# Kernel optimization log

Hardware: AMD Instinct MI355X
Metric: run time of the kernel (lower is better)

## Reference

```python
import jax, jax.numpy as jnp
import numpy as np

HIDDEN = 2048
VOCAB = 50257


def setup_inputs() -> dict:
    key = jax.random.key(0)
    ks = jax.random.split(key, 9)
    s = 0.02
    return {
        "token": jax.random.randint(ks[0], (1,), 0, VOCAB, dtype=jnp.int32),
        "hidden": jax.random.normal(ks[1], (1, 1, HIDDEN), dtype=jnp.float32),
        "emb": jax.random.normal(ks[2], (VOCAB, HIDDEN), dtype=jnp.float32) * s,
        "w_ih": jax.random.normal(ks[3], (3 * HIDDEN, HIDDEN), dtype=jnp.float32) * s,
        "w_hh": jax.random.normal(ks[4], (3 * HIDDEN, HIDDEN), dtype=jnp.float32) * s,
        "b_ih": jax.random.normal(ks[5], (3 * HIDDEN,), dtype=jnp.float32) * s,
        "b_hh": jax.random.normal(ks[6], (3 * HIDDEN,), dtype=jnp.float32) * s,
        "w_out": jax.random.normal(ks[7], (VOCAB, HIDDEN), dtype=jnp.float32) * s,
        "b_out": jax.random.normal(ks[8], (VOCAB,), dtype=jnp.float32) * s,
    }


def reference(token, hidden, emb, w_ih, w_hh, b_ih, b_hh, w_out, b_out):
    # embedding lookup + view(1,1,-1) + ReLU  -> x: [H]
    x = jax.nn.relu(emb[token].reshape(-1))
    h = hidden.reshape(-1)  # [H]
    # single GRU step (PyTorch gate order: r, z, n; separate input/hidden biases)
    gi = w_ih @ x + b_ih  # [3H]
    gh = w_hh @ h + b_hh  # [3H]
    i_r, i_z, i_n = jnp.split(gi, 3)
    h_r, h_z, h_n = jnp.split(gh, 3)
    r = jax.nn.sigmoid(i_r + h_r)
    z = jax.nn.sigmoid(i_z + h_z)
    n = jnp.tanh(i_n + r * h_n)
    h_new = (1.0 - z) * n + z * h  # [H]
    # output projection + log-softmax over vocab (dim=1 of [1, V])
    logits = w_out @ h_new + b_out  # [V]
    out = jax.nn.log_softmax(logits)[None, :]  # [1, V]
    return out, h_new.reshape(1, 1, -1)
```

## Files before the change

### kernel.cpp

```cpp
#include <hip/hip_runtime.h>
#include <math.h>

#define H 2048
#define G 6144
#define V 50257

#define WS_HNEW  0
#define WS_LOGIT 2048
#define WS_PMAX  53248
#define WS_PSUM  53376
#define NPART    128
#define NB2      6283
#define WS_PMAX2 53248
#define WS_PSUM2 59648
#define WS_FUSED_END 66048

typedef float f4 __attribute__((ext_vector_type(4)));

__device__ __forceinline__ float waveReduceSum(float v) {
  #pragma unroll
  for (int off = 32; off > 0; off >>= 1) v += __shfl_down(v, off, 64);
  return v;
}
__device__ __forceinline__ float waveReduceMax(float v) {
  #pragma unroll
  for (int off = 32; off > 0; off >>= 1) v = fmaxf(v, __shfl_down(v, off, 64));
  return v;
}
__device__ __forceinline__ float sigmoidf(float x) {
  return 1.f / (1.f + expf(-x));
}

__global__ __launch_bounds__(256) void gru_kernel(
    const int* __restrict__ token, const float* __restrict__ hidden,
    const float* __restrict__ emb, const float* __restrict__ w_ih,
    const float* __restrict__ w_hh, const float* __restrict__ b_ih,
    const float* __restrict__ b_hh, float* __restrict__ ws,
    float* __restrict__ out) {
  const int wave = threadIdx.x >> 6;
  const int lane = threadIdx.x & 63;
  const int li   = wave >> 1;
  const int side = wave & 1;
  const int i = blockIdx.x * 2 + li;
  __shared__ float sums[2][2][3];

  const f4* v4 = side ? (const f4*)hidden
                      : (const f4*)(emb + (size_t)token[0] * H);
  const float* wmat = side ? w_hh : w_ih;
  const f4* w_r = (const f4*)(wmat + (size_t)i * H);
  const f4* w_z = (const f4*)(wmat + (size_t)(H + i) * H);
  const f4* w_n = (const f4*)(wmat + (size_t)(2 * H + i) * H);

  float sr = 0.f, sz = 0.f, sn = 0.f;
  #pragma unroll
  for (int k = 0; k < 8; ++k) {
    const int idx = k * 64 + lane;
    f4 xv = v4[idx];
    if (!side) {
      xv.x = fmaxf(xv.x, 0.f); xv.y = fmaxf(xv.y, 0.f);
      xv.z = fmaxf(xv.z, 0.f); xv.w = fmaxf(xv.w, 0.f);
    }
    f4 a;
    a = w_r[idx]; sr += a.x*xv.x + a.y*xv.y + a.z*xv.z + a.w*xv.w;
    a = w_z[idx]; sz += a.x*xv.x + a.y*xv.y + a.z*xv.z + a.w*xv.w;
    a = w_n[idx]; sn += a.x*xv.x + a.y*xv.y + a.z*xv.z + a.w*xv.w;
  }
  sr = waveReduceSum(sr);
  sz = waveReduceSum(sz);
  sn = waveReduceSum(sn);
  if (lane == 0) {
    sums[li][side][0] = sr;
    sums[li][side][1] = sz;
    sums[li][side][2] = sn;
  }
  __syncthreads();
  if (side == 0 && lane == 0) {
    const float s_ir = sums[li][0][0], s_hr = sums[li][1][0];
    const float s_iz = sums[li][0][1], s_hz = sums[li][1][1];
    const float s_in = sums[li][0][2], s_hn = sums[li][1][2];
    const float r = sigmoidf(s_ir + b_ih[i] + s_hr + b_hh[i]);
    const float z = sigmoidf(s_iz + b_ih[H + i] + s_hz + b_hh[H + i]);
    const float n = tanhf(s_in + b_ih[2 * H + i] + r * (s_hn + b_hh[2 * H + i]));
    const float hn = (1.f - z) * n + z * hidden[i];
    ws[WS_HNEW + i] = hn;
    out[V + i] = hn;
  }
}

__global__ __launch_bounds__(256) void logits_kernel(
    const float* __restrict__ w_out, const float* __restrict__ b_out,
    float* __restrict__ ws, int write_partials) {
  const int wave = threadIdx.x >> 6;
  const int lane = threadIdx.x & 63;
  const int row0 = blockIdx.x * 8 + wave * 2;
  const int valid0 = (row0 < V);
  const int valid1 = (row0 + 1 < V);
  const int r0 = valid0 ? row0 : 0;
  const int r1 = valid1 ? row0 + 1 : 0;

  const f4* h4 = (const f4*)(ws + WS_HNEW);
  f4 hv[8];
  #pragma unroll
  for (int k = 0; k < 8; ++k) hv[k] = h4[k * 64 + lane];

  const f4* w0 = (const f4*)(w_out + (size_t)r0 * H);
  const f4* w1 = (const f4*)(w_out + (size_t)r1 * H);
  float s0 = 0.f, s1 = 0.f;
  #pragma unroll
  for (int k = 0; k < 8; ++k) {
    const int idx = k * 64 + lane;
    f4 a0 = __builtin_nontemporal_load(w0 + idx);
    f4 a1 = __builtin_nontemporal_load(w1 + idx);
    s0 += a0.x*hv[k].x + a0.y*hv[k].y + a0.z*hv[k].z + a0.w*hv[k].w;
    s1 += a1.x*hv[k].x + a1.y*hv[k].y + a1.z*hv[k].z + a1.w*hv[k].w;
  }
  s0 = waveReduceSum(s0);
  s1 = waveReduceSum(s1);

  __shared__ float lv[8];
  if (lane == 0) {
    const float l0 = s0 + b_out[r0];
    const float l1 = s1 + b_out[r1];
    lv[wave * 2]     = valid0 ? l0 : -INFINITY;
    lv[wave * 2 + 1] = valid1 ? l1 : -INFINITY;
    if (valid0) ws[WS_LOGIT + row0] = l0;
    if (valid1) ws[WS_LOGIT + row0 + 1] = l1;
  }
  if (!write_partials) return;
  __syncthreads();
  if (threadIdx.x == 0) {
    float m = -INFINITY;
    #pragma unroll
    for (int j = 0; j < 8; ++j) m = fmaxf(m, lv[j]);
    float s = 0.f;
    #pragma unroll
    for (int j = 0; j < 8; ++j) s += expf(lv[j] - m);
    ws[WS_PMAX2 + blockIdx.x] = m;
    ws[WS_PSUM2 + blockIdx.x] = s;
  }
}

__global__ __launch_bounds__(256) void writeout_big_kernel(
    const float* __restrict__ ws, float* __restrict__ out, int nb) {
  __shared__ float sred[4];
  __shared__ float sM, sLse;
  const int wave = threadIdx.x >> 6;
  const int lane = threadIdx.x & 63;
  float m = -INFINITY;
  for (int j = threadIdx.x; j < nb; j += 256) m = fmaxf(m, ws[WS_PMAX2 + j]);
  m = waveReduceMax(m);
  if (lane == 0) sred[wave] = m;
  __syncthreads();
  if (threadIdx.x == 0)
    sM = fmaxf(fmaxf(sred[0], sred[1]), fmaxf(sred[2], sred[3]));
  __syncthreads();
  const float M = sM;
  float s = 0.f;
  for (int j = threadIdx.x; j < nb; j += 256)
    s += ws[WS_PSUM2 + j] * expf(ws[WS_PMAX2 + j] - M);
  s = waveReduceSum(s);
  __syncthreads();
  if (lane == 0) sred[wave] = s;
  __syncthreads();
  if (threadIdx.x == 0)
    sLse = M + logf(sred[0] + sred[1] + sred[2] + sred[3]);
  __syncthreads();
  const float lse = sLse;
  const int i = blockIdx.x * 256 + threadIdx.x;
  if (i < V) out[i] = ws[WS_LOGIT + i] - lse;
}

__global__ __launch_bounds__(256) void partial_kernel(float* __restrict__ ws) {
  __shared__ float sred[4];
  __shared__ float sbmax;
  const int wave = threadIdx.x >> 6;
  const int lane = threadIdx.x & 63;
  float m = -INFINITY;
  for (int i = blockIdx.x * 256 + threadIdx.x; i < V; i += NPART * 256)
    m = fmaxf(m, ws[WS_LOGIT + i]);
  m = waveReduceMax(m);
  if (lane == 0) sred[wave] = m;
  __syncthreads();
  if (threadIdx.x == 0)
    sbmax = fmaxf(fmaxf(sred[0], sred[1]), fmaxf(sred[2], sred[3]));
  __syncthreads();
  const float M = sbmax;
  float s = 0.f;
  for (int i = blockIdx.x * 256 + threadIdx.x; i < V; i += NPART * 256)
    s += expf(ws[WS_LOGIT + i] - M);
  s = waveReduceSum(s);
  __syncthreads();
  if (lane == 0) sred[wave] = s;
  __syncthreads();
  if (threadIdx.x == 0) {
    ws[WS_PMAX + blockIdx.x] = M;
    ws[WS_PSUM + blockIdx.x] = sred[0] + sred[1] + sred[2] + sred[3];
  }
}

__global__ __launch_bounds__(256) void writeout_kernel(
    const float* __restrict__ ws, float* __restrict__ out) {
  __shared__ float pm[NPART], psv[NPART];
  __shared__ float sM[2], sS[2];
  __shared__ float sLse;
  const int tid = threadIdx.x;
  if (tid < NPART) {
    pm[tid]  = ws[WS_PMAX + tid];
    psv[tid] = ws[WS_PSUM + tid];
  }
  __syncthreads();
  if (tid < NPART) {
    float m = waveReduceMax(pm[tid]);
    if ((tid & 63) == 0) sM[tid >> 6] = m;
  }
  __syncthreads();
  const float M = fmaxf(sM[0], sM[1]);
  if (tid < NPART) {
    float e = psv[tid] * expf(pm[tid] - M);
    e = waveReduceSum(e);
    if ((tid & 63) == 0) sS[tid >> 6] = e;
  }
  __syncthreads();
  if (tid == 0) sLse = M + logf(sS[0] + sS[1]);
  __syncthreads();
  const float lse = sLse;
  const int i = blockIdx.x * 256 + tid;
  if (i < V) out[i] = ws[WS_LOGIT + i] - lse;
}

extern "C" void kernel_launch(void* const* d_in, const int* in_sizes, int n_in,
                              void* d_out, int out_size, void* d_ws, size_t ws_size,
                              hipStream_t stream) {
  const int*   token  = (const int*)  d_in[0];
  const float* hidden = (const float*)d_in[1];
  const float* emb    = (const float*)d_in[2];
  const float* w_ih   = (const float*)d_in[3];
  const float* w_hh   = (const float*)d_in[4];
  const float* b_ih   = (const float*)d_in[5];
  const float* b_hh   = (const float*)d_in[6];
  const float* w_out  = (const float*)d_in[7];
  const float* b_out  = (const float*)d_in[8];
  float* out = (float*)d_out;
  float* ws  = (float*)d_ws;

  const int fused = (ws_size >= (size_t)WS_FUSED_END * sizeof(float));

  gru_kernel<<<H / 2, 256, 0, stream>>>(token, hidden, emb, w_ih, w_hh,
                                        b_ih, b_hh, ws, out);
  logits_kernel<<<NB2, 256, 0, stream>>>(w_out, b_out, ws, fused);
  if (fused) {
    writeout_big_kernel<<<(V + 255) / 256, 256, 0, stream>>>(ws, out, NB2);
  } else {
    partial_kernel<<<NPART, 256, 0, stream>>>(ws);
    writeout_kernel<<<(V + 255) / 256, 256, 0, stream>>>(ws, out);
  }
}
```

Baseline: 744.7 us.

## Fuse log-softmax finalize into logits kernel via last-block atomic counter

The logits kernel now processes 16 rows per block (4 per wave) and drops the nontemporal loads. After each block writes its partial max and sum, it increments an atomic counter, and the last block merges all partials with an online max/sum and writes the normalized output with vectorized stores. This removes the separate writeout launch. In exchange, the final write of all 50K outputs runs on a single block.

```diff
diff --git a/kernel.cpp b/kernel.cpp
--- a/kernel.cpp
+++ b/kernel.cpp
@@ -2,18 +2,19 @@
 #include <math.h>
 
 #define H 2048
-#define G 6144
 #define V 50257
+#define RPB 16
+#define NB2 ((V + RPB - 1) / RPB)
+#define NPART 128
 
 #define WS_HNEW  0
 #define WS_LOGIT 2048
 #define WS_PMAX  53248
 #define WS_PSUM  53376
-#define NPART    128
-#define NB2      6283
 #define WS_PMAX2 53248
-#define WS_PSUM2 59648
-#define WS_FUSED_END 66048
+#define WS_PSUM2 56448
+#define WS_CNT   59648
+#define WS_END   59712
 
 typedef float f4 __attribute__((ext_vector_type(4)));
 
@@ -37,6 +38,7 @@
     const float* __restrict__ w_hh, const float* __restrict__ b_ih,
     const float* __restrict__ b_hh, float* __restrict__ ws,
     float* __restrict__ out) {
+  if (blockIdx.x == 0 && threadIdx.x == 0) *(int*)(ws + WS_CNT) = 0;
   const int wave = threadIdx.x >> 6;
   const int lane = threadIdx.x & 63;
   const int li   = wave >> 1;
@@ -87,87 +89,119 @@
   }
 }
 
-__global__ __launch_bounds__(256) void logits_kernel(
+__global__ __launch_bounds__(256, 4) void logits_kernel(
     const float* __restrict__ w_out, const float* __restrict__ b_out,
-    float* __restrict__ ws, int write_partials) {
+    float* __restrict__ ws, float* __restrict__ out, int fused) {
   const int wave = threadIdx.x >> 6;
   const int lane = threadIdx.x & 63;
-  const int row0 = blockIdx.x * 8 + wave * 2;
-  const int valid0 = (row0 < V);
-  const int valid1 = (row0 + 1 < V);
-  const int r0 = valid0 ? row0 : 0;
-  const int r1 = valid1 ? row0 + 1 : 0;
+  const int row0 = blockIdx.x * RPB + wave * 4;
+  int   r[4];
+  int   valid[4];
+  #pragma unroll
+  for (int j = 0; j < 4; ++j) {
+    valid[j] = (row0 + j < V);
+    r[j] = valid[j] ? row0 + j : 0;
+  }
 
   const f4* h4 = (const f4*)(ws + WS_HNEW);
   f4 hv[8];
   #pragma unroll
   for (int k = 0; k < 8; ++k) hv[k] = h4[k * 64 + lane];
 
-  const f4* w0 = (const f4*)(w_out + (size_t)r0 * H);
-  const f4* w1 = (const f4*)(w_out + (size_t)r1 * H);
-  float s0 = 0.f, s1 = 0.f;
+  const f4* wp0 = (const f4*)(w_out + (size_t)r[0] * H);
+  const f4* wp1 = (const f4*)(w_out + (size_t)r[1] * H);
+  const f4* wp2 = (const f4*)(w_out + (size_t)r[2] * H);
+  const f4* wp3 = (const f4*)(w_out + (size_t)r[3] * H);
+  float s0 = 0.f, s1 = 0.f, s2 = 0.f, s3 = 0.f;
   #pragma unroll
   for (int k = 0; k < 8; ++k) {
     const int idx = k * 64 + lane;
-    f4 a0 = __builtin_nontemporal_load(w0 + idx);
-    f4 a1 = __builtin_nontemporal_load(w1 + idx);
+    f4 a0 = wp0[idx];
+    f4 a1 = wp1[idx];
+    f4 a2 = wp2[idx];
+    f4 a3 = wp3[idx];
     s0 += a0.x*hv[k].x + a0.y*hv[k].y + a0.z*hv[k].z + a0.w*hv[k].w;
     s1 += a1.x*hv[k].x + a1.y*hv[k].y + a1.z*hv[k].z + a1.w*hv[k].w;
+    s2 += a2.x*hv[k].x + a2.y*hv[k].y + a2.z*hv[k].z + a2.w*hv[k].w;
+    s3 += a3.x*hv[k].x + a3.y*hv[k].y + a3.z*hv[k].z + a3.w*hv[k].w;
   }
   s0 = waveReduceSum(s0);
   s1 = waveReduceSum(s1);
-
-  __shared__ float lv[8];
+  s2 = waveReduceSum(s2);
+  s3 = waveReduceSum(s3);
+
+  __shared__ float lv[RPB];
   if (lane == 0) {
-    const float l0 = s0 + b_out[r0];
-    const float l1 = s1 + b_out[r1];
-    lv[wave * 2]     = valid0 ? l0 : -INFINITY;
-    lv[wave * 2 + 1] = valid1 ? l1 : -INFINITY;
-    if (valid0) ws[WS_LOGIT + row0] = l0;
-    if (valid1) ws[WS_LOGIT + row0 + 1] = l1;
-  }
-  if (!write_partials) return;
-  __syncthreads();
+    float sv[4] = {s0, s1, s2, s3};
+    #pragma unroll
+    for (int j = 0; j < 4; ++j) {
+      const float l = sv[j] + b_out[r[j]];
+      lv[wave * 4 + j] = valid[j] ? l : -INFINITY;
+      if (valid[j]) ws[WS_LOGIT + row0 + j] = l;
+    }
+  }
+  if (!fused) return;
+  __syncthreads();
+
+  __shared__ int sLast;
   if (threadIdx.x == 0) {
     float m = -INFINITY;
     #pragma unroll
-    for (int j = 0; j < 8; ++j) m = fmaxf(m, lv[j]);
-    float s = 0.f;
-    #pragma unroll
-    for (int j = 0; j < 8; ++j) s += expf(lv[j] - m);
+    for (int j = 0; j < RPB; ++j) m = fmaxf(m, lv[j]);
+    float ss = 0.f;
+    #pragma unroll
+    for (int j = 0; j < RPB; ++j) ss += expf(lv[j] - m);
     ws[WS_PMAX2 + blockIdx.x] = m;
-    ws[WS_PSUM2 + blockIdx.x] = s;
-  }
-}
-
-__global__ __launch_bounds__(256) void writeout_big_kernel(
-    const float* __restrict__ ws, float* __restrict__ out, int nb) {
-  __shared__ float sred[4];
-  __shared__ float sM, sLse;
-  const int wave = threadIdx.x >> 6;
-  const int lane = threadIdx.x & 63;
-  float m = -INFINITY;
-  for (int j = threadIdx.x; j < nb; j += 256) m = fmaxf(m, ws[WS_PMAX2 + j]);
-  m = waveReduceMax(m);
-  if (lane == 0) sred[wave] = m;
-  __syncthreads();
-  if (threadIdx.x == 0)
-    sM = fmaxf(fmaxf(sred[0], sred[1]), fmaxf(sred[2], sred[3]));
-  __syncthreads();
-  const float M = sM;
-  float s = 0.f;
-  for (int j = threadIdx.x; j < nb; j += 256)
-    s += ws[WS_PSUM2 + j] * expf(ws[WS_PMAX2 + j] - M);
-  s = waveReduceSum(s);
-  __syncthreads();
-  if (lane == 0) sred[wave] = s;
-  __syncthreads();
-  if (threadIdx.x == 0)
-    sLse = M + logf(sred[0] + sred[1] + sred[2] + sred[3]);
+    ws[WS_PSUM2 + blockIdx.x] = ss;
+    __threadfence();
+    const int old = atomicAdd((int*)(ws + WS_CNT), 1);
+    sLast = (old == NB2 - 1);
+  }
+  __syncthreads();
+  if (!sLast) return;
+
+  __threadfence();
+  float m = -INFINITY, ss = 0.f;
+  for (int j = threadIdx.x; j < NB2; j += 256) {
+    const float pm = ws[WS_PMAX2 + j];
+    const float ps = ws[WS_PSUM2 + j];
+    const float nm = fmaxf(m, pm);
+    ss = ss * expf(m - nm) + ps * expf(pm - nm);
+    m = nm;
+  }
+  #pragma unroll
+  for (int off = 32; off > 0; off >>= 1) {
+    const float m2 = __shfl_down(m, off, 64);
+    const float ss2 = __shfl_down(ss, off, 64);
+    const float nm = fmaxf(m, m2);
+    ss = ss * expf(m - nm) + ss2 * expf(m2 - nm);
+    m = nm;
+  }
+  __shared__ float redM[4], redS[4];
+  __shared__ float sLse;
+  if (lane == 0) { redM[wave] = m; redS[wave] = ss; }
+  __syncthreads();
+  if (threadIdx.x == 0) {
+    float M = -INFINITY, S = 0.f;
+    #pragma unroll
+    for (int w = 0; w < 4; ++w) {
+      const float nm = fmaxf(M, redM[w]);
+      S = S * expf(M - nm) + redS[w] * expf(redM[w] - nm);
+      M = nm;
+    }
+    sLse = M + logf(S);
+  }
   __syncthreads();
   const float lse = sLse;
-  const int i = blockIdx.x * 256 + threadIdx.x;
-  if (i < V) out[i] = ws[WS_LOGIT + i] - lse;
+  const int nvec = V / 4;
+  const f4* lg4 = (const f4*)(ws + WS_LOGIT);
+  f4* out4 = (f4*)out;
+  for (int j = threadIdx.x; j < nvec; j += 256) {
+    f4 l = lg4[j];
+    f4 o = {l.x - lse, l.y - lse, l.z - lse, l.w - lse};
+    out4[j] = o;
+  }
+  if (threadIdx.x == 0) out[V - 1] = ws[WS_LOGIT + V - 1] - lse;
 }
 
 __global__ __launch_bounds__(256) void partial_kernel(float* __restrict__ ws) {
@@ -243,14 +277,12 @@
   float* out = (float*)d_out;
   float* ws  = (float*)d_ws;
 
-  const int fused = (ws_size >= (size_t)WS_FUSED_END * sizeof(float));
+  const int fused = (ws_size >= (size_t)WS_END * sizeof(float));
 
   gru_kernel<<<H / 2, 256, 0, stream>>>(token, hidden, emb, w_ih, w_hh,
                                         b_ih, b_hh, ws, out);
-  logits_kernel<<<NB2, 256, 0, stream>>>(w_out, b_out, ws, fused);
-  if (fused) {
-    writeout_big_kernel<<<(V + 255) / 256, 256, 0, stream>>>(ws, out, NB2);
-  } else {
+  logits_kernel<<<NB2, 256, 0, stream>>>(w_out, b_out, ws, out, fused);
+  if (!fused) {
     partial_kernel<<<NPART, 256, 0, stream>>>(ws);
     writeout_kernel<<<(V + 255) / 256, 256, 0, stream>>>(ws, out);
   }
```

Result: slower. 922.7 us (+23.9%).
